# Optimization experiments

Measured on AMD Instinct MI355X. Metric: run time of the kernel, lower is better.

The kernel has to match this reference:

```python
import jax, jax.numpy as jnp
import numpy as np

H = 16  # heads (query_heads == kv_heads in this config)
LN_EPS = 1e-5


def setup_inputs() -> dict:
    key = jax.random.key(0)
    ks = jax.random.split(key, 6)
    B, T, C = 4, 1024, 1024
    s = lambda fan_in: 1.0 / np.sqrt(fan_in)
    return {
        "x": jax.random.normal(ks[0], (B, T, C), jnp.float32),
        "c_attn_w": jax.random.normal(ks[1], (C, 3 * C), jnp.float32) * s(C),
        "c_attn_b": jnp.zeros((3 * C,), jnp.float32),
        "q_w": jax.random.normal(ks[2], (C, C), jnp.float32) * s(C),
        "q_b": jnp.zeros((C,), jnp.float32),
        "k_w": jax.random.normal(ks[3], (C, C), jnp.float32) * s(C),
        "k_b": jnp.zeros((C,), jnp.float32),
        "v_w": jax.random.normal(ks[4], (C, C), jnp.float32) * s(C),
        "v_b": jnp.zeros((C,), jnp.float32),
        "ln_g": jnp.ones((C,), jnp.float32),
        "ln_b": jnp.zeros((C,), jnp.float32),
        "out_w": jax.random.normal(ks[5], (C, C), jnp.float32) * s(C),
        "out_b": jnp.zeros((C,), jnp.float32),
    }


def reference(x, c_attn_w, c_attn_b, q_w, q_b, k_w, k_b, v_w, v_b,
              ln_g, ln_b, out_w, out_b):
    B, T, C = x.shape
    d = C // H
    # c_attn then split into query/key/value streams
    qkv = x @ c_attn_w + c_attn_b            # [B,T,3C]
    query, key_, value = jnp.split(qkv, 3, axis=-1)
    q = query @ q_w + q_b                     # [B,T,C]
    k = key_ @ k_w + k_b
    v = value @ v_w + v_b
    # split heads: b n (h d) -> b h n d
    q = q.reshape(B, T, H, d).transpose(0, 2, 1, 3)
    k = k.reshape(B, T, H, d).transpose(0, 2, 1, 3)
    v = v.reshape(B, T, H, d).transpose(0, 2, 1, 3)
    scale = d ** 0.5
    # NOTE: original code scales query by 1/scale AND the similarity by 1/scale
    # (net 1/d). Preserved faithfully.
    sim = jnp.einsum("bhnd,bhsd->bhns", q / scale, k)  # [B,H,T,T]
    causal = jnp.tril(jnp.ones((T, T), dtype=bool))
    sim = jnp.where(causal, sim, jnp.finfo(sim.dtype).min)
    attn = jax.nn.softmax(sim / scale, axis=-1)
    o = jnp.einsum("bhns,bhsd->bnhd", attn, v).reshape(B, T, C)
    # LayerNorm (eps=1e-5)
    mu = jnp.mean(o, axis=-1, keepdims=True)
    var = jnp.var(o, axis=-1, keepdims=True)
    o = (o - mu) * jax.lax.rsqrt(var + LN_EPS) * ln_g + ln_b
    return o @ out_w + out_b
```

## Files before the change

### kernel.cpp

```cpp
#include <hip/hip_runtime.h>
#include <hip/hip_bf16.h>
#include <stdint.h>

typedef __bf16 bf16_t;
typedef bf16_t bf16x4 __attribute__((ext_vector_type(4)));
typedef bf16_t bf16x8 __attribute__((ext_vector_type(8)));
typedef float  f32x4  __attribute__((ext_vector_type(4)));

#define B_   4
#define T_   1024
#define C_   1024
#define H_   16

__device__ __forceinline__ f32x4 mfma_bf16(bf16x8 a, bf16x8 b, f32x4 c) {
  return __builtin_amdgcn_mfma_f32_16x16x32_bf16(a, b, c, 0, 0, 0);
}

__device__ __forceinline__ void async16(const bf16_t* g, bf16_t* l) {
  __builtin_amdgcn_global_load_lds(
      (__attribute__((address_space(1))) void*)(uintptr_t)g,
      (__attribute__((address_space(3))) void*)l, 16, 0, 0);
}

__global__ __launch_bounds__(256) void convert2_f32_bf16(
    const float* __restrict__ a, bf16_t* __restrict__ oa, int na4,
    const float* __restrict__ b, bf16_t* __restrict__ ob, int nb4)
{
  const int i = blockIdx.x * 256 + threadIdx.x;
  const float* src; bf16_t* dst; int idx;
  if (i < na4) { src = a; dst = oa; idx = i; }
  else if (i < na4 + nb4) { src = b; dst = ob; idx = i - na4; }
  else return;
  const float4 v = *(const float4*)(src + (size_t)idx * 4);
  bf16x4 o;
  o[0] = (bf16_t)v.x; o[1] = (bf16_t)v.y; o[2] = (bf16_t)v.z; o[3] = (bf16_t)v.w;
  *(bf16x4*)(dst + (size_t)idx * 4) = o;
}

__global__ __launch_bounds__(256) void transpose4_f32_bf16(
    const float* __restrict__ a0, const float* __restrict__ a1,
    const float* __restrict__ a2, const float* __restrict__ a3,
    const float* __restrict__ lng, bf16_t* __restrict__ out)
{
  __shared__ bf16_t tile[32][33];
  const int z = blockIdx.z;
  const float* in = (z == 0) ? a0 : (z == 1) ? a1 : (z == 2) ? a2 : a3;
  bf16_t* o = out + ((size_t)z << 20);
  const int n0 = blockIdx.x * 32, k0 = blockIdx.y * 32;
  const int x = threadIdx.x & 31, y4 = (threadIdx.x >> 5) * 4;
#pragma unroll
  for (int i = 0; i < 4; ++i) {
    float v = in[(size_t)(k0 + y4 + i) * 1024 + n0 + x];
    if (z == 3) v *= lng[k0 + y4 + i];
    tile[y4 + i][x] = (bf16_t)v;
  }
  __syncthreads();
#pragma unroll
  for (int i = 0; i < 4; ++i)
    o[(size_t)(n0 + y4 + i) * 1024 + k0 + x] = tile[x][y4 + i];
}

__global__ __launch_bounds__(256) void transpose_v(
    const bf16_t* __restrict__ qkvb, bf16_t* __restrict__ vfrag)
{
  __shared__ bf16_t tile[64][66];
  const int bid = blockIdx.x;
  const int kb = bid & 15, bh = bid >> 4;
  const int b = bh >> 4, h = bh & 15;
  const int t = threadIdx.x;
  {
    const int key = t & 63, fc = (t >> 6) * 16;
    const bf16_t* src =
        qkvb + (size_t)(b * 1024 + kb * 64 + key) * 3072 + 2048 + h * 64 + fc;
    bf16x8 v0 = *(const bf16x8*)src;
    bf16x8 v1 = *(const bf16x8*)(src + 8);
#pragma unroll
    for (int j = 0; j < 8; ++j) {
      tile[fc + j][key]     = v0[j];
      tile[fc + 8 + j][key] = v1[j];
    }
  }
  __syncthreads();
#pragma unroll
  for (int ww = 0; ww < 2; ++ww) {
    const int g = t * 2 + ww;
    const int chunk = g >> 6;
    const int lane2 = g & 63;
    const int lr2 = lane2 & 15, lg2 = lane2 >> 4;
    const int kk = chunk >> 2, nf = chunk & 3;
    const int f = nf * 16 + lr2;
    const int key0 = kk * 32 + lg2 * 8;
    bf16x8 val;
#pragma unroll
    for (int j = 0; j < 8; ++j) val[j] = tile[f][key0 + j];
    *(bf16x8*)&vfrag[(((size_t)bh * 16 + kb) * 8 + chunk) * 512 + lane2 * 8] = val;
  }
}

__global__ __launch_bounds__(256) void prep_vec_kernel(
    const float* __restrict__ cb,
    const float* __restrict__ w0, const float* __restrict__ w1,
    const float* __restrict__ w2,
    const float* __restrict__ b0, const float* __restrict__ b1,
    const float* __restrict__ b2,
    const float* __restrict__ ow, const float* __restrict__ lng,
    const float* __restrict__ lnb, const float* __restrict__ outb,
    float* __restrict__ out_qkv, float* __restrict__ svec,
    float* __restrict__ c2v, float* __restrict__ ssum, float* __restrict__ ssq)
{
  const int bid = blockIdx.x;
  if (bid >= 80) {
    const float4 z = {0.f, 0.f, 0.f, 0.f};
#pragma unroll
    for (int k = 0; k < 4; ++k) {
      ((float4*)ssum)[threadIdx.x * 4 + k] = z;
      ((float4*)ssq)[threadIdx.x * 4 + k] = z;
    }
    return;
  }
  __shared__ float part[4][64];
  const int jl = threadIdx.x & 63, cq = threadIdx.x >> 6;
  const int c0 = cq * 256;
  if (bid < 48) {
    const int j = bid * 64 + jl;
    const int s = j >> 10, jj = j & 1023;
    const float* w  = (s == 0) ? w0 : (s == 1) ? w1 : w2;
    const float* sb = (s == 0) ? b0 : (s == 1) ? b1 : b2;
    float acc = 0.f;
#pragma unroll 8
    for (int c = c0; c < c0 + 256; ++c)
      acc += cb[s * 1024 + c] * w[(size_t)c * 1024 + jj];
    part[cq][jl] = acc;
    __syncthreads();
    if (cq == 0)
      out_qkv[j] = part[0][jl] + part[1][jl] + part[2][jl] + part[3][jl] + sb[jj];
  } else {
    const int jj = (bid - 48) * 64 + jl;
    const int col = jj & 1023;
    const float* coef = (jj < 1024) ? lng : lnb;
    float acc = 0.f;
#pragma unroll 8
    for (int c = c0; c < c0 + 256; ++c)
      acc += coef[c] * ow[(size_t)c * 1024 + col];
    part[cq][jl] = acc;
    __syncthreads();
    if (cq == 0) {
      const float tot = part[0][jl] + part[1][jl] + part[2][jl] + part[3][jl];
      if (jj < 1024) svec[col] = tot;
      else           c2v[col] = tot + outb[col];
    }
  }
}

template <typename OT>
__global__ __launch_bounds__(256) void gemm_bt_bias(
    const bf16_t* __restrict__ A, int lda,
    const bf16_t* __restrict__ Bt, int ldb,
    const float* __restrict__ bias,
    OT* __restrict__ C, int ldc,
    int K, int nTilesN, int blocksPerMat,
    int strideA, int strideB, int strideC, int xcdSwz)
{
  __shared__ __align__(16) bf16_t As[3][128 * 32];
  __shared__ __align__(16) bf16_t Bs[3][128 * 32];
  int raw = blockIdx.x;
  if (xcdSwz) {
    const int cpx = gridDim.x >> 3;
    raw = (raw & 7) * cpx + (raw >> 3);
  }
  const int s   = raw / blocksPerMat;
  const int bid = raw % blocksPerMat;
  A  += (size_t)s * strideA;
  Bt += (size_t)s * strideB;
  C  += (size_t)s * strideC;
  const int mt = bid / nTilesN, nt = bid % nTilesN;
  const int m0 = mt * 128, n0 = nt * 128;
  const int tid = threadIdx.x;
  const int lane = tid & 63;
  const int lr = lane & 15, lg = lane >> 4;
  const int wid = tid >> 6;
  const int wr = wid >> 1, wc = wid & 1;
  const int sLg = lg ^ ((lr >> 1) & 3);

  f32x4 acc[4][4];
#pragma unroll
  for (int m = 0; m < 4; ++m)
#pragma unroll
    for (int n = 0; n < 4; ++n) acc[m][n] = (f32x4){0.f, 0.f, 0.f, 0.f};

  const int nk = K >> 5;

  auto stage = [&](int buf, int t) {
    const int k0 = t << 5;
#pragma unroll
    for (int p = 0; p < 2; ++p) {
      const int c = p * 256 + tid;
      const int row = c >> 2;
      const int col = (((c & 3) ^ ((c >> 3) & 3)) << 3);
      async16(A + (size_t)(m0 + row) * lda + k0 + col, &As[buf][c * 8]);
      async16(Bt + (size_t)(n0 + row) * ldb + k0 + col, &Bs[buf][c * 8]);
    }
  };

  stage(0, 0);
  stage(1, 1);
  asm volatile("s_waitcnt vmcnt(4)" ::: "memory");
  __builtin_amdgcn_sched_barrier(0);
  __builtin_amdgcn_s_barrier();
  __builtin_amdgcn_sched_barrier(0);

  for (int t = 0; t < nk; ++t) {
    const int buf = t % 3;
    if (t + 2 < nk) stage((t + 2) % 3, t + 2);

    bf16x8 af[4], bfr[4];
#pragma unroll
    for (int m = 0; m < 4; ++m)
      af[m] = *(const bf16x8*)&As[buf][(wr * 64 + m * 16 + lr) * 32 + sLg * 8];
#pragma unroll
    for (int n = 0; n < 4; ++n)
      bfr[n] = *(const bf16x8*)&Bs[buf][(wc * 64 + n * 16 + lr) * 32 + sLg * 8];

    if (t + 2 < nk)
      asm volatile("s_waitcnt lgkmcnt(0) vmcnt(4)" ::: "memory");
    else
      asm volatile("s_waitcnt lgkmcnt(0) vmcnt(0)" ::: "memory");
    __builtin_amdgcn_sched_barrier(0);
    __builtin_amdgcn_s_barrier();
    __builtin_amdgcn_sched_barrier(0);

    __builtin_amdgcn_s_setprio(1);
#pragma unroll
    for (int m = 0; m < 4; ++m)
#pragma unroll
      for (int n = 0; n < 4; ++n)
        acc[m][n] = mfma_bf16(af[m], bfr[n], acc[m][n]);
    __builtin_amdgcn_s_setprio(0);
  }

#pragma unroll
  for (int n = 0; n < 4; ++n) {
    const int col = n0 + wc * 64 + n * 16 + lr;
    const float bv = bias ? bias[col] : 0.0f;
#pragma unroll
    for (int m = 0; m < 4; ++m) {
      const int row = m0 + wr * 64 + m * 16 + lg * 4;
#pragma unroll
      for (int r = 0; r < 4; ++r)
        C[(size_t)(row + r) * ldc + col] = (OT)(acc[m][n][r] + bv);
    }
  }
}

__global__ __launch_bounds__(256) void gemm_ln(
    const bf16_t* __restrict__ A, int lda,
    const bf16_t* __restrict__ Bt, int ldb,
    const float* __restrict__ svec, const float* __restrict__ c2v,
    const float* __restrict__ ssum, const float* __restrict__ ssq,
    float* __restrict__ C, int ldc, int K, int nTilesN)
{
  __shared__ __align__(16) bf16_t As[3][128 * 32];
  __shared__ __align__(16) bf16_t Bs[3][128 * 32];
  int raw = blockIdx.x;
  {
    const int cpx = gridDim.x >> 3;
    raw = (raw & 7) * cpx + (raw >> 3);
  }
  const int mt = raw / nTilesN, nt = raw % nTilesN;
  const int m0 = mt * 128, n0 = nt * 128;
  const int tid = threadIdx.x;
  const int lane = tid & 63;
  const int lr = lane & 15, lg = lane >> 4;
  const int wid = tid >> 6;
  const int wr = wid >> 1, wc = wid & 1;
  const int sLg = lg ^ ((lr >> 1) & 3);

  f32x4 acc[4][4];
#pragma unroll
  for (int m = 0; m < 4; ++m)
#pragma unroll
    for (int n = 0; n < 4; ++n) acc[m][n] = (f32x4){0.f, 0.f, 0.f, 0.f};

  const int nk = K >> 5;

  auto stage = [&](int buf, int t) {
    const int k0 = t << 5;
#pragma unroll
    for (int p = 0; p < 2; ++p) {
      const int c = p * 256 + tid;
      const int row = c >> 2;
      const int col = (((c & 3) ^ ((c >> 3) & 3)) << 3);
      async16(A + (size_t)(m0 + row) * lda + k0 + col, &As[buf][c * 8]);
      async16(Bt + (size_t)(n0 + row) * ldb + k0 + col, &Bs[buf][c * 8]);
    }
  };

  stage(0, 0);
  stage(1, 1);
  asm volatile("s_waitcnt vmcnt(4)" ::: "memory");
  __builtin_amdgcn_sched_barrier(0);
  __builtin_amdgcn_s_barrier();
  __builtin_amdgcn_sched_barrier(0);

  for (int t = 0; t < nk; ++t) {
    const int buf = t % 3;
    if (t + 2 < nk) stage((t + 2) % 3, t + 2);

    bf16x8 af[4], bfr[4];
#pragma unroll
    for (int m = 0; m < 4; ++m)
      af[m] = *(const bf16x8*)&As[buf][(wr * 64 + m * 16 + lr) * 32 + sLg * 8];
#pragma unroll
    for (int n = 0; n < 4; ++n)
      bfr[n] = *(const bf16x8*)&Bs[buf][(wc * 64 + n * 16 + lr) * 32 + sLg * 8];

    if (t + 2 < nk)
      asm volatile("s_waitcnt lgkmcnt(0) vmcnt(4)" ::: "memory");
    else
      asm volatile("s_waitcnt lgkmcnt(0) vmcnt(0)" ::: "memory");
    __builtin_amdgcn_sched_barrier(0);
    __builtin_amdgcn_s_barrier();
    __builtin_amdgcn_sched_barrier(0);

    __builtin_amdgcn_s_setprio(1);
#pragma unroll
    for (int m = 0; m < 4; ++m)
#pragma unroll
      for (int n = 0; n < 4; ++n)
        acc[m][n] = mfma_bf16(af[m], bfr[n], acc[m][n]);
    __builtin_amdgcn_s_setprio(0);
  }

#pragma unroll
  for (int n = 0; n < 4; ++n) {
    const int col = n0 + wc * 64 + n * 16 + lr;
    const float sj = svec[col];
    const float c2 = c2v[col];
#pragma unroll
    for (int m = 0; m < 4; ++m) {
      const int row = m0 + wr * 64 + m * 16 + lg * 4;
      const float* s1 = &ssum[row];
      const float* s2 = &ssq[row];
#pragma unroll
      for (int r = 0; r < 4; ++r) {
        const float mu  = s1[r] * (1.0f / 1024.0f);
        const float var = s2[r] * (1.0f / 1024.0f) - mu * mu;
        const float al  = rsqrtf(var + 1e-5f);
        C[(size_t)(row + r) * ldc + col] = al * acc[m][n][r] - al * mu * sj + c2;
      }
    }
  }
}

__global__ __launch_bounds__(256) void attn_kernel(
    const bf16_t* __restrict__ qkv, const bf16_t* __restrict__ vfrag,
    bf16_t* __restrict__ o, float* __restrict__ ssum, float* __restrict__ ssq)
{
  __shared__ __align__(16) bf16_t Ks[2][8][512];
  __shared__ __align__(16) bf16_t Vs[2][8][512];
  __shared__ __align__(16) bf16_t Ps[4][16][72];
  const int LD = 3072;
  const bf16_t* q = qkv;
  const bf16_t* k = qkv + 1024;

  const int raw = blockIdx.x;
  const int xcd = raw & 7, idx = raw >> 3;
  const int bh   = (idx >> 3) * 8 + xcd;
  const int slot = idx & 7;
  const int b = bh >> 4, h = bh & 15;

  const int tid = threadIdx.x;
  const int lane = tid & 63;
  const int lr = lane & 15, lg = lane >> 4;
  const int w = tid >> 6;

  const bf16_t* kbase = k + (size_t)(b * T_) * LD + h * 64;
  const bf16_t* vfbase = vfrag + (size_t)bh * 16 * 8 * 512;

  auto stage = [&](int bf, int it) {
    const int kv0 = it << 6;
#pragma unroll
    for (int cc = 0; cc < 4; ++cc) {
      const int c = w * 4 + cc;
      if (c < 8) {
        const int kg = c >> 1, kk = c & 1;
        async16(kbase + (size_t)(kv0 + kg * 16 + lr) * LD + kk * 32 + lg * 8,
                &Ks[bf][c][lane * 8]);
      } else {
        const int cv = c - 8;
        async16(vfbase + ((size_t)it * 8 + cv) * 512 + lane * 8,
                &Vs[bf][cv][lane * 8]);
      }
    }
  };

#pragma unroll
  for (int pass = 0; pass < 2; ++pass) {
    const int band = pass ? (15 - slot) : slot;
    const int myq = band * 64 + w * 16 + lr;
    const int nIter = band + 1;

    bf16x8 qf[2];
    {
      const size_t qr = (size_t)(b * T_ + myq) * LD + h * 64;
      qf[0] = *(const bf16x8*)&q[qr + lg * 8];
      qf[1] = *(const bf16x8*)&q[qr + 32 + lg * 8];
    }

    float mi = -3.0e38f, li = 0.0f;
    f32x4 acc[4];
#pragma unroll
    for (int nf = 0; nf < 4; ++nf) acc[nf] = (f32x4){0.f, 0.f, 0.f, 0.f};

    stage(0, 0);
    __syncthreads();

    for (int it = 0; it < nIter; ++it) {
      const int bf = it & 1;
      if (it + 1 < nIter) stage(bf ^ 1, it + 1);
      const int kv0 = it << 6;

      f32x4 sfr[4];
      __builtin_amdgcn_s_setprio(1);
#pragma unroll
      for (int kg = 0; kg < 4; ++kg) {
        bf16x8 kf0 = *(const bf16x8*)&Ks[bf][kg * 2 + 0][lane * 8];
        bf16x8 kf1 = *(const bf16x8*)&Ks[bf][kg * 2 + 1][lane * 8];
        f32x4 z = (f32x4){0.f, 0.f, 0.f, 0.f};
        z = mfma_bf16(kf0, qf[0], z);
        z = mfma_bf16(kf1, qf[1], z);
        sfr[kg] = z;
      }
      __builtin_amdgcn_s_setprio(0);

      float sv[4][4];
      float pm[4];
#pragma unroll
      for (int kg = 0; kg < 4; ++kg) {
        const int keyb = kv0 + kg * 16 + lg * 4;
        pm[kg] = -3.0e38f;
#pragma unroll
        for (int r = 0; r < 4; ++r) {
          float xx = sfr[kg][r] * 0.015625f;
          if (keyb + r > myq) xx = -3.0e38f;
          sv[kg][r] = xx;
          pm[kg] = fmaxf(pm[kg], xx);
        }
      }
      float pmax = fmaxf(fmaxf(pm[0], pm[1]), fmaxf(pm[2], pm[3]));
      pmax = fmaxf(pmax, __shfl_xor(pmax, 16));
      pmax = fmaxf(pmax, __shfl_xor(pmax, 32));
      const float mnew = fmaxf(mi, pmax);
      const float fr = __expf(mi - mnew);
      mi = mnew;
      float ps[4];
#pragma unroll
      for (int kg = 0; kg < 4; ++kg) {
        float p0 = __expf(sv[kg][0] - mi);
        float p1 = __expf(sv[kg][1] - mi);
        float p2 = __expf(sv[kg][2] - mi);
        float p3 = __expf(sv[kg][3] - mi);
        sv[kg][0] = p0; sv[kg][1] = p1; sv[kg][2] = p2; sv[kg][3] = p3;
        ps[kg] = (p0 + p1) + (p2 + p3);
      }
      float psum = (ps[0] + ps[1]) + (ps[2] + ps[3]);
      psum += __shfl_xor(psum, 16);
      psum += __shfl_xor(psum, 32);
      li = li * fr + psum;
#pragma unroll
      for (int nf = 0; nf < 4; ++nf)
#pragma unroll
        for (int r = 0; r < 4; ++r) acc[nf][r] *= fr;

#pragma unroll
      for (int kg = 0; kg < 4; ++kg) {
        bf16x4 p4;
#pragma unroll
        for (int r = 0; r < 4; ++r) p4[r] = (bf16_t)sv[kg][r];
        *(bf16x4*)&Ps[w][lr][kg * 16 + lg * 4] = p4;
      }

      __builtin_amdgcn_s_setprio(1);
#pragma unroll
      for (int kk = 0; kk < 2; ++kk) {
        bf16x8 pf = *(const bf16x8*)&Ps[w][lr][kk * 32 + lg * 8];
#pragma unroll
        for (int nf = 0; nf < 4; ++nf) {
          bf16x8 vf = *(const bf16x8*)&Vs[bf][kk * 4 + nf][lane * 8];
          acc[nf] = mfma_bf16(vf, pf, acc[nf]);
        }
      }
      __builtin_amdgcn_s_setprio(0);

      __syncthreads();
    }

    const float inv = 1.0f / li;
    float st1 = 0.f, st2 = 0.f;
#pragma unroll
    for (int nf = 0; nf < 4; ++nf) {
      bf16x4 o4;
#pragma unroll
      for (int r = 0; r < 4; ++r) {
        const float ov = acc[nf][r] * inv;
        o4[r] = (bf16_t)ov;
        st1 += ov;
        st2 += ov * ov;
      }
      *(bf16x4*)&o[(size_t)(b * T_ + myq) * C_ + h * 64 + nf * 16 + lg * 4] = o4;
    }
    st1 += __shfl_xor(st1, 16); st1 += __shfl_xor(st1, 32);
    st2 += __shfl_xor(st2, 16); st2 += __shfl_xor(st2, 32);
    if (lg == 0) {
      atomicAdd(&ssum[b * T_ + myq], st1);
      atomicAdd(&ssq[b * T_ + myq], st2);
    }
  }
}

extern "C" void kernel_launch(void* const* d_in, const int* in_sizes, int n_in,
                              void* d_out, int out_size, void* d_ws, size_t ws_size,
                              hipStream_t stream)
{
  const float* x        = (const float*)d_in[0];
  const float* c_attn_w = (const float*)d_in[1];
  const float* c_attn_b = (const float*)d_in[2];
  const float* q_w      = (const float*)d_in[3];
  const float* q_b      = (const float*)d_in[4];
  const float* k_w      = (const float*)d_in[5];
  const float* k_b      = (const float*)d_in[6];
  const float* v_w      = (const float*)d_in[7];
  const float* v_b      = (const float*)d_in[8];
  const float* ln_g     = (const float*)d_in[9];
  const float* ln_b     = (const float*)d_in[10];
  const float* out_w    = (const float*)d_in[11];
  const float* out_b    = (const float*)d_in[12];

  char* ws = (char*)d_ws;
  bf16_t* qkvb      = (bf16_t*)(ws + 0);
  bf16_t* xb        = (bf16_t*)(ws + 25165824);
  bf16_t* ob        = (bf16_t*)(ws + 25165824);
  bf16_t* WsT4      = (bf16_t*)(ws + 33554432);
  bf16_t* c_attn_wb = (bf16_t*)(ws + 41943040);
  bf16_t* Wt_eff    = (bf16_t*)(ws + 48234496);
  float*  bias_eff  = (float*)(ws + 54525952);
  bf16_t* vfrag     = (bf16_t*)(ws + 54538240);
  float*  ssum      = (float*)(ws + 62926848);
  float*  ssq       = (float*)(ws + 62943232);
  float*  svec      = (float*)(ws + 62959616);
  float*  c2v       = (float*)(ws + 62963712);

  convert2_f32_bf16<<<dim3(7168), 256, 0, stream>>>(
      x, xb, 1048576, c_attn_w, c_attn_wb, 786432);

  transpose4_f32_bf16<<<dim3(32, 32, 4), 256, 0, stream>>>(
      q_w, k_w, v_w, out_w, ln_g, WsT4);

  gemm_bt_bias<bf16_t><<<dim3(192), 256, 0, stream>>>(
      WsT4, 1024, c_attn_wb, 3072, nullptr, Wt_eff, 1024,
      1024, 8, 64, 1 << 20, 1024, 1 << 20, 0);

  prep_vec_kernel<<<dim3(81), 256, 0, stream>>>(
      c_attn_b, q_w, k_w, v_w, q_b, k_b, v_b,
      out_w, ln_g, ln_b, out_b, bias_eff, svec, c2v, ssum, ssq);

  gemm_bt_bias<bf16_t><<<dim3(768), 256, 0, stream>>>(
      xb, 1024, Wt_eff, 1024, bias_eff, qkvb, 3072, 1024, 24, 768, 0, 0, 0, 1);

  transpose_v<<<dim3(1024), 256, 0, stream>>>(qkvb, vfrag);

  attn_kernel<<<dim3(512), 256, 0, stream>>>(qkvb, vfrag, ob, ssum, ssq);

  gemm_ln<<<dim3(256), 256, 0, stream>>>(
      ob, 1024, WsT4 + (size_t)3 * (1 << 20), 1024,
      svec, c2v, ssum, ssq, (float*)d_out, 1024, 1024, 8);
}
```

Baseline: 154.0 us.

## Fuse prep kernels into one launch and use smaller tiles for weight-fold GEMM

Folds the fp32→bf16 convert, weight transposes, and bias/LN-vector prep into a single kernel dispatched by block index, which cuts launch overhead and lets independent prep work run concurrently. The gemm is templated on tile size, and the weight-folding GEMM (3 x 1024x1024) now uses 64x64 tiles with 768 blocks and XCD swizzle instead of 192 blocks of 128x128, so more CUs are filled. Smaller tiles cost more operand reloads per FLOP, and the fused kernel needs shared memory for both branches.

```diff
diff --git a/kernel.cpp b/kernel.cpp
--- a/kernel.cpp
+++ b/kernel.cpp
@@ -22,42 +22,96 @@
       (__attribute__((address_space(3))) void*)l, 16, 0, 0);
 }
 
-__global__ __launch_bounds__(256) void convert2_f32_bf16(
-    const float* __restrict__ a, bf16_t* __restrict__ oa, int na4,
-    const float* __restrict__ b, bf16_t* __restrict__ ob, int nb4)
-{
-  const int i = blockIdx.x * 256 + threadIdx.x;
-  const float* src; bf16_t* dst; int idx;
-  if (i < na4) { src = a; dst = oa; idx = i; }
-  else if (i < na4 + nb4) { src = b; dst = ob; idx = i - na4; }
-  else return;
-  const float4 v = *(const float4*)(src + (size_t)idx * 4);
-  bf16x4 o;
-  o[0] = (bf16_t)v.x; o[1] = (bf16_t)v.y; o[2] = (bf16_t)v.z; o[3] = (bf16_t)v.w;
-  *(bf16x4*)(dst + (size_t)idx * 4) = o;
-}
-
-__global__ __launch_bounds__(256) void transpose4_f32_bf16(
-    const float* __restrict__ a0, const float* __restrict__ a1,
-    const float* __restrict__ a2, const float* __restrict__ a3,
-    const float* __restrict__ lng, bf16_t* __restrict__ out)
+__global__ __launch_bounds__(256) void prep_all(
+    const float* __restrict__ x, bf16_t* __restrict__ xb,
+    const float* __restrict__ caw, bf16_t* __restrict__ cawb,
+    const float* __restrict__ qw, const float* __restrict__ kw,
+    const float* __restrict__ vw, const float* __restrict__ ow,
+    const float* __restrict__ lng, bf16_t* __restrict__ WsT4,
+    const float* __restrict__ cb,
+    const float* __restrict__ qb, const float* __restrict__ kb,
+    const float* __restrict__ vb,
+    const float* __restrict__ lnb, const float* __restrict__ outb,
+    float* __restrict__ out_qkv, float* __restrict__ svec,
+    float* __restrict__ c2v, float* __restrict__ ssum, float* __restrict__ ssq)
 {
   __shared__ bf16_t tile[32][33];
-  const int z = blockIdx.z;
-  const float* in = (z == 0) ? a0 : (z == 1) ? a1 : (z == 2) ? a2 : a3;
-  bf16_t* o = out + ((size_t)z << 20);
-  const int n0 = blockIdx.x * 32, k0 = blockIdx.y * 32;
-  const int x = threadIdx.x & 31, y4 = (threadIdx.x >> 5) * 4;
-#pragma unroll
-  for (int i = 0; i < 4; ++i) {
-    float v = in[(size_t)(k0 + y4 + i) * 1024 + n0 + x];
-    if (z == 3) v *= lng[k0 + y4 + i];
-    tile[y4 + i][x] = (bf16_t)v;
-  }
-  __syncthreads();
-#pragma unroll
-  for (int i = 0; i < 4; ++i)
-    o[(size_t)(n0 + y4 + i) * 1024 + k0 + x] = tile[x][y4 + i];
+  __shared__ float part[4][64];
+  const int bid = blockIdx.x;
+  const int tid = threadIdx.x;
+
+  if (bid < 7168) {
+    const int i = bid * 256 + tid;
+    const float* src; bf16_t* dst; int idx;
+    if (i < 1048576) { src = x; dst = xb; idx = i; }
+    else { src = caw; dst = cawb; idx = i - 1048576; }
+    const float4 v = *(const float4*)(src + (size_t)idx * 4);
+    bf16x4 o;
+    o[0] = (bf16_t)v.x; o[1] = (bf16_t)v.y; o[2] = (bf16_t)v.z; o[3] = (bf16_t)v.w;
+    *(bf16x4*)(dst + (size_t)idx * 4) = o;
+    return;
+  }
+  if (bid < 11264) {
+    const int b2 = bid - 7168;
+    const int z = b2 >> 10, rem = b2 & 1023;
+    const int bx = rem & 31, by = rem >> 5;
+    const float* in = (z == 0) ? qw : (z == 1) ? kw : (z == 2) ? vw : ow;
+    bf16_t* o = WsT4 + ((size_t)z << 20);
+    const int n0 = bx * 32, k0 = by * 32;
+    const int xl = tid & 31, y4 = (tid >> 5) * 4;
+#pragma unroll
+    for (int i = 0; i < 4; ++i) {
+      float v = in[(size_t)(k0 + y4 + i) * 1024 + n0 + xl];
+      if (z == 3) v *= lng[k0 + y4 + i];
+      tile[y4 + i][xl] = (bf16_t)v;
+    }
+    __syncthreads();
+#pragma unroll
+    for (int i = 0; i < 4; ++i)
+      o[(size_t)(n0 + y4 + i) * 1024 + k0 + xl] = tile[xl][y4 + i];
+    return;
+  }
+  const int pbid = bid - 11264;
+  if (pbid >= 80) {
+    const float4 z4 = {0.f, 0.f, 0.f, 0.f};
+#pragma unroll
+    for (int k = 0; k < 4; ++k) {
+      ((float4*)ssum)[tid * 4 + k] = z4;
+      ((float4*)ssq)[tid * 4 + k] = z4;
+    }
+    return;
+  }
+  const int jl = tid & 63, cq = tid >> 6;
+  const int c0 = cq * 256;
+  if (pbid < 48) {
+    const int j = pbid * 64 + jl;
+    const int s = j >> 10, jj = j & 1023;
+    const float* w  = (s == 0) ? qw : (s == 1) ? kw : vw;
+    const float* sb = (s == 0) ? qb : (s == 1) ? kb : vb;
+    float acc = 0.f;
+#pragma unroll 8
+    for (int c = c0; c < c0 + 256; ++c)
+      acc += cb[s * 1024 + c] * w[(size_t)c * 1024 + jj];
+    part[cq][jl] = acc;
+    __syncthreads();
+    if (cq == 0)
+      out_qkv[j] = part[0][jl] + part[1][jl] + part[2][jl] + part[3][jl] + sb[jj];
+  } else {
+    const int jj = (pbid - 48) * 64 + jl;
+    const int col = jj & 1023;
+    const float* coef = (jj < 1024) ? lng : lnb;
+    float acc = 0.f;
+#pragma unroll 8
+    for (int c = c0; c < c0 + 256; ++c)
+      acc += coef[c] * ow[(size_t)c * 1024 + col];
+    part[cq][jl] = acc;
+    __syncthreads();
+    if (cq == 0) {
+      const float tot = part[0][jl] + part[1][jl] + part[2][jl] + part[3][jl];
+      if (jj < 1024) svec[col] = tot;
+      else           c2v[col] = tot + outb[col];
+    }
+  }
 }
 
 __global__ __launch_bounds__(256) void transpose_v(
@@ -97,62 +151,7 @@
   }
 }
 
-__global__ __launch_bounds__(256) void prep_vec_kernel(
-    const float* __restrict__ cb,
-    const float* __restrict__ w0, const float* __restrict__ w1,
-    const float* __restrict__ w2,
-    const float* __restrict__ b0, const float* __restrict__ b1,
-    const float* __restrict__ b2,
-    const float* __restrict__ ow, const float* __restrict__ lng,
-    const float* __restrict__ lnb, const float* __restrict__ outb,
-    float* __restrict__ out_qkv, float* __restrict__ svec,
-    float* __restrict__ c2v, float* __restrict__ ssum, float* __restrict__ ssq)
-{
-  const int bid = blockIdx.x;
-  if (bid >= 80) {
-    const float4 z = {0.f, 0.f, 0.f, 0.f};
-#pragma unroll
-    for (int k = 0; k < 4; ++k) {
-      ((float4*)ssum)[threadIdx.x * 4 + k] = z;
-      ((float4*)ssq)[threadIdx.x * 4 + k] = z;
-    }
-    return;
-  }
-  __shared__ float part[4][64];
-  const int jl = threadIdx.x & 63, cq = threadIdx.x >> 6;
-  const int c0 = cq * 256;
-  if (bid < 48) {
-    const int j = bid * 64 + jl;
-    const int s = j >> 10, jj = j & 1023;
-    const float* w  = (s == 0) ? w0 : (s == 1) ? w1 : w2;
-    const float* sb = (s == 0) ? b0 : (s == 1) ? b1 : b2;
-    float acc = 0.f;
-#pragma unroll 8
-    for (int c = c0; c < c0 + 256; ++c)
-      acc += cb[s * 1024 + c] * w[(size_t)c * 1024 + jj];
-    part[cq][jl] = acc;
-    __syncthreads();
-    if (cq == 0)
-      out_qkv[j] = part[0][jl] + part[1][jl] + part[2][jl] + part[3][jl] + sb[jj];
-  } else {
-    const int jj = (bid - 48) * 64 + jl;
-    const int col = jj & 1023;
-    const float* coef = (jj < 1024) ? lng : lnb;
-    float acc = 0.f;
-#pragma unroll 8
-    for (int c = c0; c < c0 + 256; ++c)
-      acc += coef[c] * ow[(size_t)c * 1024 + col];
-    part[cq][jl] = acc;
-    __syncthreads();
-    if (cq == 0) {
-      const float tot = part[0][jl] + part[1][jl] + part[2][jl] + part[3][jl];
-      if (jj < 1024) svec[col] = tot;
-      else           c2v[col] = tot + outb[col];
-    }
-  }
-}
-
-template <typename OT>
+template <typename OT, int TM, int TN>
 __global__ __launch_bounds__(256) void gemm_bt_bias(
     const bf16_t* __restrict__ A, int lda,
     const bf16_t* __restrict__ Bt, int ldb,
@@ -161,8 +160,10 @@
     int K, int nTilesN, int blocksPerMat,
     int strideA, int strideB, int strideC, int xcdSwz)
 {
-  __shared__ __align__(16) bf16_t As[3][128 * 32];
-  __shared__ __align__(16) bf16_t Bs[3][128 * 32];
+  constexpr int TILEM = 32 * TM, TILEN = 32 * TN;
+  constexpr int LPS = TM / 2 + TN / 2;
+  __shared__ __align__(16) bf16_t As[3][TILEM * 32];
+  __shared__ __align__(16) bf16_t Bs[3][TILEN * 32];
   int raw = blockIdx.x;
   if (xcdSwz) {
     const int cpx = gridDim.x >> 3;
@@ -174,7 +175,7 @@
   Bt += (size_t)s * strideB;
   C  += (size_t)s * strideC;
   const int mt = bid / nTilesN, nt = bid % nTilesN;
-  const int m0 = mt * 128, n0 = nt * 128;
+  const int m0 = mt * TILEM, n0 = nt * TILEN;
   const int tid = threadIdx.x;
   const int lane = tid & 63;
   const int lr = lane & 15, lg = lane >> 4;
@@ -182,29 +183,38 @@
   const int wr = wid >> 1, wc = wid & 1;
   const int sLg = lg ^ ((lr >> 1) & 3);
 
-  f32x4 acc[4][4];
-#pragma unroll
-  for (int m = 0; m < 4; ++m)
-#pragma unroll
-    for (int n = 0; n < 4; ++n) acc[m][n] = (f32x4){0.f, 0.f, 0.f, 0.f};
+  f32x4 acc[TM][TN];
+#pragma unroll
+  for (int m = 0; m < TM; ++m)
+#pragma unroll
+    for (int n = 0; n < TN; ++n) acc[m][n] = (f32x4){0.f, 0.f, 0.f, 0.f};
 
   const int nk = K >> 5;
 
   auto stage = [&](int buf, int t) {
     const int k0 = t << 5;
 #pragma unroll
-    for (int p = 0; p < 2; ++p) {
+    for (int p = 0; p < TM / 2; ++p) {
       const int c = p * 256 + tid;
       const int row = c >> 2;
       const int col = (((c & 3) ^ ((c >> 3) & 3)) << 3);
       async16(A + (size_t)(m0 + row) * lda + k0 + col, &As[buf][c * 8]);
+    }
+#pragma unroll
+    for (int p = 0; p < TN / 2; ++p) {
+      const int c = p * 256 + tid;
+      const int row = c >> 2;
+      const int col = (((c & 3) ^ ((c >> 3) & 3)) << 3);
       async16(Bt + (size_t)(n0 + row) * ldb + k0 + col, &Bs[buf][c * 8]);
     }
   };
 
   stage(0, 0);
   stage(1, 1);
-  asm volatile("s_waitcnt vmcnt(4)" ::: "memory");
+  if constexpr (LPS == 4)
+    asm volatile("s_waitcnt vmcnt(4)" ::: "memory");
+  else
+    asm volatile("s_waitcnt vmcnt(2)" ::: "memory");
   __builtin_amdgcn_sched_barrier(0);
   __builtin_amdgcn_s_barrier();
   __builtin_amdgcn_sched_barrier(0);
@@ -213,38 +223,44 @@
     const int buf = t % 3;
     if (t + 2 < nk) stage((t + 2) % 3, t + 2);
 
-    bf16x8 af[4], bfr[4];
-#pragma unroll
-    for (int m = 0; m < 4; ++m)
-      af[m] = *(const bf16x8*)&As[buf][(wr * 64 + m * 16 + lr) * 32 + sLg * 8];
-#pragma unroll
-    for (int n = 0; n < 4; ++n)
-      bfr[n] = *(const bf16x8*)&Bs[buf][(wc * 64 + n * 16 + lr) * 32 + sLg * 8];
-
-    if (t + 2 < nk)
-      asm volatile("s_waitcnt lgkmcnt(0) vmcnt(4)" ::: "memory");
-    else
+    bf16x8 af[TM], bfr[TN];
+#pragma unroll
+    for (int m = 0; m < TM; ++m)
+      af[m] = *(const bf16x8*)
+          &As[buf][(wr * TM * 16 + m * 16 + lr) * 32 + sLg * 8];
+#pragma unroll
+    for (int n = 0; n < TN; ++n)
+      bfr[n] = *(const bf16x8*)
+          &Bs[buf][(wc * TN * 16 + n * 16 + lr) * 32 + sLg * 8];
+
+    if (t + 2 < nk) {
+      if constexpr (LPS == 4)
+        asm volatile("s_waitcnt lgkmcnt(0) vmcnt(4)" ::: "memory");
+      else
+        asm volatile("s_waitcnt lgkmcnt(0) vmcnt(2)" ::: "memory");
+    } else {
       asm volatile("s_waitcnt lgkmcnt(0) vmcnt(0)" ::: "memory");
+    }
     __builtin_amdgcn_sched_barrier(0);
     __builtin_amdgcn_s_barrier();
     __builtin_amdgcn_sched_barrier(0);
 
     __builtin_amdgcn_s_setprio(1);
 #pragma unroll
-    for (int m = 0; m < 4; ++m)
-#pragma unroll
-      for (int n = 0; n < 4; ++n)
+    for (int m = 0; m < TM; ++m)
+#pragma unroll
+      for (int n = 0; n < TN; ++n)
         acc[m][n] = mfma_bf16(af[m], bfr[n], acc[m][n]);
     __builtin_amdgcn_s_setprio(0);
   }
 
 #pragma unroll
-  for (int n = 0; n < 4; ++n) {
-    const int col = n0 + wc * 64 + n * 16 + lr;
+  for (int n = 0; n < TN; ++n) {
+    const int col = n0 + wc * TN * 16 + n * 16 + lr;
     const float bv = bias ? bias[col] : 0.0f;
 #pragma unroll
-    for (int m = 0; m < 4; ++m) {
-      const int row = m0 + wr * 64 + m * 16 + lg * 4;
+    for (int m = 0; m < TM; ++m) {
+      const int row = m0 + wr * TM * 16 + m * 16 + lg * 4;
 #pragma unroll
       for (int r = 0; r < 4; ++r)
         C[(size_t)(row + r) * ldc + col] = (OT)(acc[m][n][r] + bv);
@@ -550,21 +566,17 @@
   float*  svec      = (float*)(ws + 62959616);
   float*  c2v       = (float*)(ws + 62963712);
 
-  convert2_f32_bf16<<<dim3(7168), 256, 0, stream>>>(
-      x, xb, 1048576, c_attn_w, c_attn_wb, 786432);
-
-  transpose4_f32_bf16<<<dim3(32, 32, 4), 256, 0, stream>>>(
-      q_w, k_w, v_w, out_w, ln_g, WsT4);
-
-  gemm_bt_bias<bf16_t><<<dim3(192), 256, 0, stream>>>(
+  prep_all<<<dim3(11345), 256, 0, stream>>>(
+      x, xb, c_attn_w, c_attn_wb,
+      q_w, k_w, v_w, out_w, ln_g, WsT4,
+      c_attn_b, q_b, k_b, v_b, ln_b, out_b,
+      bias_eff, svec, c2v, ssum, ssq);
+
+  gemm_bt_bias<bf16_t, 2, 2><<<dim3(768), 256, 0, stream>>>(
       WsT4, 1024, c_attn_wb, 3072, nullptr, Wt_eff, 1024,
-      1024, 8, 64, 1 << 20, 1024, 1 << 20, 0);
-
-  prep_vec_kernel<<<dim3(81), 256, 0, stream>>>(
-      c_attn_b, q_w, k_w, v_w, q_b, k_b, v_b,
-      out_w, ln_g, ln_b, out_b, bias_eff, svec, c2v, ssum, ssq);
-
-  gemm_bt_bias<bf16_t><<<dim3(768), 256, 0, stream>>>(
+      1024, 16, 256, 1 << 20, 1024, 1 << 20, 1);
+
+  gemm_bt_bias<bf16_t, 4, 4><<<dim3(768), 256, 0, stream>>>(
       xb, 1024, Wt_eff, 1024, bias_eff, qkvb, 3072, 1024, 24, 768, 0, 0, 0, 1);
 
   transpose_v<<<dim3(1024), 256, 0, stream>>>(qkvb, vfrag);
```

After: 143.0 us. 1.08x faster.
